# Kernel optimization log

Measured on AMD Instinct MI355X. Metric: run time of the kernel, lower is better.

## Reference

```python
import jax, jax.numpy as jnp
import numpy as np

WS = 512   # window_size
LB = 1     # look_backward
LF = 1     # look_forward
H = 16     # num_attention_heads
NC = LB + LF + 1  # concatenated windows per query window


def _collect(a, pad_value):
    # a: [B, nw, ws, ...]; gather windows [i-LB, i+LF] for each window i,
    # padding the window axis with pad_value (faithful to collect_windows).
    nw = a.shape[1]
    pads = [(0, 0), (LB, LF)] + [(0, 0)] * (a.ndim - 2)
    ap = jnp.pad(a, pads, constant_values=pad_value)
    idx = jnp.arange(nw)[:, None] + jnp.arange(NC)[None, :]  # [nw, NC]
    g = ap[:, idx]  # [B, nw, NC, ws, ...]
    return g.reshape(g.shape[0], nw, NC * a.shape[2], *a.shape[3:])


def setup_inputs() -> dict:
    key = jax.random.key(0)
    ks = jax.random.split(key, 9)
    B, S, E = 1, 4096, 1024
    x = jax.random.normal(ks[0], (B, S, E), dtype=jnp.float32)
    std = 0.02
    wq = std * jax.random.normal(ks[1], (E, E), dtype=jnp.float32)
    wk = std * jax.random.normal(ks[2], (E, E), dtype=jnp.float32)
    wv = std * jax.random.normal(ks[3], (E, E), dtype=jnp.float32)
    wo = std * jax.random.normal(ks[4], (E, E), dtype=jnp.float32)
    bq = std * jax.random.normal(ks[5], (E,), dtype=jnp.float32)
    bk = std * jax.random.normal(ks[6], (E,), dtype=jnp.float32)
    bv = std * jax.random.normal(ks[7], (E,), dtype=jnp.float32)
    bo = std * jax.random.normal(ks[8], (E,), dtype=jnp.float32)
    return {"x": x, "wq": wq, "bq": bq, "wk": wk, "bk": bk,
            "wv": wv, "bv": bv, "wo": wo, "bo": bo}


def reference(x, wq, bq, wk, bk, wv, bv, wo, bo):
    B, S, E = x.shape
    hd = E // H
    nw = S // WS  # seq_len chosen divisible by window_size

    def proj(w, b):
        y = x @ w.T + b
        return y.reshape(B, S, H, hd).transpose(0, 2, 1, 3).reshape(B * H, S, hd)

    q = proj(wq, bq)
    k = proj(wk, bk)
    v = proj(wv, bv)

    qb = q.reshape(B * H, nw, WS, hd)
    # NOTE: original pads K/V window buffers with value -1 (not zero); pad
    # positions are NOT masked (the `!= -1` clause excludes them) -- replicated.
    kb = _collect(k.reshape(B * H, nw, WS, hd), -1.0)  # [BH, nw, NC*WS, hd]
    vb = _collect(v.reshape(B * H, nw, WS, hd), -1.0)

    t = jnp.arange(S, dtype=jnp.int32).reshape(1, nw, WS)
    ct = _collect(t, -1)  # [1, nw, NC*WS] key positions (-1 for pads)

    # Unscaled QK^T (original applies no 1/sqrt(d)).
    scores = jnp.einsum('bwqd,bwkd->bwqk', qb, kb)  # [BH, nw, WS, NC*WS]

    qi = t.reshape(1, nw, WS, 1)          # query absolute positions
    ctb = ct[:, :, None, :]               # key absolute positions
    over = ((ctb > qi + WS * LF) | (ctb < qi - WS * LB)) & (ctb != -1)
    scores = jnp.where(over, -jnp.inf, scores)

    attn = jax.nn.softmax(scores, axis=-1)
    out = jnp.einsum('bwqk,bwkd->bwqd', attn, vb)  # [BH, nw, WS, hd]
    out = out.reshape(B, H, S, hd).transpose(0, 2, 1, 3).reshape(B, S, E)
    return out @ wo.T + bo
```

## Files before the change

### kernel.cpp

```cpp
#include <hip/hip_runtime.h>
#include <stdint.h>

#define S 4096
#define E 1024
#define NH 16
#define HD 64
#define WSZ 512

typedef _Float16 f16x8 __attribute__((ext_vector_type(8)));
typedef _Float16 f16x4 __attribute__((ext_vector_type(4)));
typedef float f32x4 __attribute__((ext_vector_type(4)));
typedef unsigned short u16;
typedef unsigned int u32;

__device__ __forceinline__ u16 f2h_bits(float f) {
    union { _Float16 h; u16 u; } cv; cv.h = (_Float16)f; return cv.u;
}

__device__ __forceinline__ void gld16(const u16* g, u16* l) {
    __builtin_amdgcn_global_load_lds((const __attribute__((address_space(1))) void*)g,
                                     (__attribute__((address_space(3))) void*)l, 16, 0, 0);
}

struct CvtArgs {
    const float* s[5];
    u16* d[5];
    int n[5];
};
__global__ void cvt5(CvtArgs a) {
    int seg = blockIdx.y;
    const float* __restrict__ s = a.s[seg];
    u16* __restrict__ d = a.d[seg];
    int n = a.n[seg];
    for (int i = (blockIdx.x * 256 + threadIdx.x) * 4; i < n; i += gridDim.x * 1024) {
        float4 f = *(const float4*)&s[i];
        uint2 o;
        o.x = (u32)f2h_bits(f.x) | ((u32)f2h_bits(f.y) << 16);
        o.y = (u32)f2h_bits(f.z) | ((u32)f2h_bits(f.w) << 16);
        *(uint2*)&d[i] = o;
    }
}

__global__ __launch_bounds__(256) void gemm_qkv(
    const u16* __restrict__ A, const u16* __restrict__ B,
    u16* __restrict__ OutQK, u16* __restrict__ OutVT,
    const float* __restrict__ b0, const float* __restrict__ b1, const float* __restrict__ b2,
    int K) {
    __shared__ __align__(16) u16 As[128 * 32];
    __shared__ __align__(16) u16 Bs[128 * 32];
    const int tid = threadIdx.x;
    const int wid = tid >> 6, lid = tid & 63, quad = lid >> 4, l16 = lid & 15;
    const int wm = wid >> 1, wn = wid & 1;
    const int bm0 = blockIdx.y * 128, bn0 = blockIdx.x * 128;

    f32x4 acc[4][4] = {};
    const int sr = tid >> 2, sc = (tid & 3) * 8;

    for (int k0 = 0; k0 < K; k0 += 32) {
        __syncthreads();
        gld16(&A[(size_t)(bm0 + sr) * K + k0 + sc],      &As[tid * 8]);
        gld16(&A[(size_t)(bm0 + sr + 64) * K + k0 + sc], &As[2048 + tid * 8]);
        gld16(&B[(size_t)(bn0 + sr) * K + k0 + sc],      &Bs[tid * 8]);
        gld16(&B[(size_t)(bn0 + sr + 64) * K + k0 + sc], &Bs[2048 + tid * 8]);
        __syncthreads();
        f16x8 af[4], bf[4];
#pragma unroll
        for (int i = 0; i < 4; ++i) af[i] = *(const f16x8*)&As[(wm * 64 + i * 16 + l16) * 32 + quad * 8];
#pragma unroll
        for (int j = 0; j < 4; ++j) bf[j] = *(const f16x8*)&Bs[(wn * 64 + j * 16 + l16) * 32 + quad * 8];
#pragma unroll
        for (int i = 0; i < 4; ++i)
#pragma unroll
            for (int j = 0; j < 4; ++j)
                acc[i][j] = __builtin_amdgcn_mfma_f32_16x16x32_f16(af[i], bf[j], acc[i][j], 0, 0, 0);
    }

    const bool isV = (bn0 >= 2048);
#pragma unroll
    for (int j = 0; j < 4; ++j) {
        int n = bn0 + wn * 64 + j * 16 + l16;
        float bias = (n < 1024) ? b0[n] : (n < 2048 ? b1[n - 1024] : b2[n - 2048]);
#pragma unroll
        for (int i = 0; i < 4; ++i) {
            int m0 = bm0 + wm * 64 + i * 16 + quad * 4;
            if (!isV) {
#pragma unroll
                for (int r = 0; r < 4; ++r)
                    OutQK[(size_t)(m0 + r) * 2048 + n] = f2h_bits(acc[i][j][r] + bias);
            } else {
                u16 h0 = f2h_bits(acc[i][j][0] + bias);
                u16 h1 = f2h_bits(acc[i][j][1] + bias);
                u16 h2 = f2h_bits(acc[i][j][2] + bias);
                u16 h3 = f2h_bits(acc[i][j][3] + bias);
                uint2 pk;
                pk.x = (u32)h0 | ((u32)h1 << 16);
                pk.y = (u32)h2 | ((u32)h3 << 16);
                *(uint2*)&OutVT[(size_t)(n - 2048) * 4096 + m0] = pk;
            }
        }
    }
}

__global__ __launch_bounds__(256) void gemm_n64(
    const u16* __restrict__ A, const u16* __restrict__ B, float* __restrict__ OutF,
    const float* __restrict__ bias, int N, int K) {
    __shared__ __align__(16) u16 As[128 * 32];
    __shared__ __align__(16) u16 Bs[64 * 32];
    const int tid = threadIdx.x;
    const int wid = tid >> 6, lid = tid & 63, quad = lid >> 4, l16 = lid & 15;
    const int bm0 = blockIdx.y * 128, bn0 = blockIdx.x * 64;

    f32x4 acc[2][4] = {};
    const int sr = tid >> 2, sc = (tid & 3) * 8;

    for (int k0 = 0; k0 < K; k0 += 32) {
        __syncthreads();
        gld16(&A[(size_t)(bm0 + sr) * K + k0 + sc],      &As[tid * 8]);
        gld16(&A[(size_t)(bm0 + sr + 64) * K + k0 + sc], &As[2048 + tid * 8]);
        gld16(&B[(size_t)(bn0 + sr) * K + k0 + sc],      &Bs[tid * 8]);
        __syncthreads();
        f16x8 af[2], bf[4];
#pragma unroll
        for (int i = 0; i < 2; ++i) af[i] = *(const f16x8*)&As[(wid * 32 + i * 16 + l16) * 32 + quad * 8];
#pragma unroll
        for (int j = 0; j < 4; ++j) bf[j] = *(const f16x8*)&Bs[(j * 16 + l16) * 32 + quad * 8];
#pragma unroll
        for (int i = 0; i < 2; ++i)
#pragma unroll
            for (int j = 0; j < 4; ++j)
                acc[i][j] = __builtin_amdgcn_mfma_f32_16x16x32_f16(af[i], bf[j], acc[i][j], 0, 0, 0);
    }

#pragma unroll
    for (int j = 0; j < 4; ++j) {
        int n = bn0 + j * 16 + l16;
        float bv = bias[n];
#pragma unroll
        for (int i = 0; i < 2; ++i) {
            int m0 = bm0 + wid * 32 + i * 16 + quad * 4;
#pragma unroll
            for (int r = 0; r < 4; ++r)
                OutF[(size_t)(m0 + r) * N + n] = acc[i][j][r] + bv;
        }
    }
}

__global__ __launch_bounds__(512, 4) void attn_win(const u16* __restrict__ QK, const u16* __restrict__ VT,
                                                   u16* __restrict__ AO) {
    const int qt = blockIdx.x, w = blockIdx.y, h = blockIdx.z;
    const int tid = threadIdx.x, wid = tid >> 6, lid = tid & 63, quad = lid >> 4, l16 = lid & 15;

    __shared__ __align__(16) u16 Ks[2][64 * 32];
    __shared__ __align__(16) u16 Vt[2][64 * 36];

    const int qrow = w * WSZ + qt * 128 + wid * 16 + l16;
    f16x8 qf[2];
#pragma unroll
    for (int ks = 0; ks < 2; ++ks)
        qf[ks] = *(const f16x8*)&QK[(size_t)qrow * 2048 + h * 64 + ks * 32 + quad * 8];

    f32x4 oacc[4] = {};
    float mrun = -30000.f;
    float lsum = 0.f;

    const int g0base = (w - 1) * WSZ;
    const int rqloc = qt * 128 + wid * 16 + l16;
    const int rqw0 = qt * 128 + wid * 16;
    const u16 NEG1 = 0xBC00;

    const int kst = tid & 255, kkh = tid >> 8;
    const int vd = tid >> 3, vk0 = (tid & 7) * 8;

    for (int c = 0; c < 24; ++c) {
        const int g0 = g0base + c * 64;
        const bool pad_chunk = (g0 < 0) || (g0 >= S);
        const bool band = (c * 64 + 63 >= qt * 128) && (c * 64 <= qt * 128 + 1151);
        if (!(pad_chunk || band)) continue;

        __syncthreads();
        if (!pad_chunk) {
            gld16(QK + (size_t)(g0 + (kst >> 2)) * 2048 + 1024 + h * 64 + kkh * 32 + (kst & 3) * 8,
                  &Ks[0][0] + kkh * 2048 + kst * 8);
            {
                uint4 va = *(const uint4*)(VT + (size_t)(h * 64 + vd) * 4096 + g0 + vk0);
                u16* vp = &Vt[vk0 >> 5][vd * 36 + (vk0 & 31)];
                *(uint2*)(vp)     = make_uint2(va.x, va.y);
                *(uint2*)(vp + 4) = make_uint2(va.z, va.w);
            }
        } else {
            {
                u32 p = ((u32)NEG1 << 16) | NEG1;
                uint4 val = make_uint4(p, p, p, p);
                *(uint4*)&Ks[kkh][(kst >> 2) * 32 + (kst & 3) * 8] = val;
                u16* vp = &Vt[vk0 >> 5][vd * 36 + (vk0 & 31)];
                *(uint2*)(vp)     = make_uint2(p, p);
                *(uint2*)(vp + 4) = make_uint2(p, p);
            }
        }
        __syncthreads();

        f32x4 sc[4];
#pragma unroll
        for (int nt = 0; nt < 4; ++nt) {
            f16x8 kf0 = *(const f16x8*)&Ks[0][(nt * 16 + l16) * 32 + quad * 8];
            f16x8 kf1 = *(const f16x8*)&Ks[1][(nt * 16 + l16) * 32 + quad * 8];
            f32x4 t = {};
            t = __builtin_amdgcn_mfma_f32_16x16x32_f16(kf0, qf[0], t, 0, 0, 0);
            t = __builtin_amdgcn_mfma_f32_16x16x32_f16(kf1, qf[1], t, 0, 0, 0);
            sc[nt] = t;
        }

        const bool needs_mask = !pad_chunk &&
            ((c * 64 < rqw0 + 16) || (c * 64 + 63 > rqw0 + 1024));
        if (needs_mask) {
#pragma unroll
            for (int nt = 0; nt < 4; ++nt)
#pragma unroll
                for (int r = 0; r < 4; ++r) {
                    int n = c * 64 + nt * 16 + quad * 4 + r;
                    if (n < rqloc || n > rqloc + 1024) sc[nt][r] = -30000.f;
                }
        }

        float mloc = mrun;
#pragma unroll
        for (int nt = 0; nt < 4; ++nt) {
            mloc = fmaxf(mloc, fmaxf(fmaxf(sc[nt][0], sc[nt][1]), fmaxf(sc[nt][2], sc[nt][3])));
        }
        mloc = fmaxf(mloc, __shfl_xor(mloc, 16, 64));
        mloc = fmaxf(mloc, __shfl_xor(mloc, 32, 64));
        float alpha = __expf(mrun - mloc);
        mrun = mloc;
        float ls = 0.f;
        f16x4 pf[4];
#pragma unroll
        for (int nt = 0; nt < 4; ++nt)
#pragma unroll
            for (int r = 0; r < 4; ++r) {
                float p = __expf(sc[nt][r] - mloc);
                ls += p;
                pf[nt][r] = (_Float16)p;
            }
        lsum = lsum * alpha + ls;
        float ao[4];
#pragma unroll
        for (int r = 0; r < 4; ++r) ao[r] = __shfl(alpha, quad * 4 + r, 64);
#pragma unroll
        for (int dt = 0; dt < 4; ++dt)
#pragma unroll
            for (int r = 0; r < 4; ++r) oacc[dt][r] *= ao[r];

#pragma unroll
        for (int nt = 0; nt < 4; ++nt)
#pragma unroll
            for (int dt = 0; dt < 4; ++dt) {
                f16x4 vf = *(const f16x4*)&Vt[nt >> 1][(dt * 16 + l16) * 36 + (nt & 1) * 16 + quad * 4];
                oacc[dt] = __builtin_amdgcn_mfma_f32_16x16x16f16(pf[nt], vf, oacc[dt], 0, 0, 0);
            }
    }

    float lt = lsum;
    lt += __shfl_xor(lt, 16, 64);
    lt += __shfl_xor(lt, 32, 64);
    float linv = 1.f / lt;
    float lrec[4];
#pragma unroll
    for (int r = 0; r < 4; ++r) lrec[r] = __shfl(linv, quad * 4 + r, 64);
#pragma unroll
    for (int dt = 0; dt < 4; ++dt)
#pragma unroll
        for (int r = 0; r < 4; ++r) {
            int srow = w * WSZ + qt * 128 + wid * 16 + quad * 4 + r;
            int col = h * 64 + dt * 16 + l16;
            AO[(size_t)srow * E + col] = f2h_bits(oacc[dt][r] * lrec[r]);
        }
}

extern "C" void kernel_launch(void* const* d_in, const int* in_sizes, int n_in,
                              void* d_out, int out_size, void* d_ws, size_t ws_size,
                              hipStream_t stream) {
    const float* x  = (const float*)d_in[0];
    const float* wq = (const float*)d_in[1];
    const float* bq = (const float*)d_in[2];
    const float* wk = (const float*)d_in[3];
    const float* bk = (const float*)d_in[4];
    const float* wv = (const float*)d_in[5];
    const float* bv = (const float*)d_in[6];
    const float* wo = (const float*)d_in[7];
    const float* bo = (const float*)d_in[8];
    float* out = (float*)d_out;

    char* ws = (char*)d_ws;
    u16* XH  = (u16*)(ws);
    u16* WC  = (u16*)(ws + 8388608);
    u16* WOh = (u16*)(ws + 14680064);
    u16* QK  = (u16*)(ws + 16777216);
    u16* VTg = (u16*)(ws + 33554432);
    u16* AOh = (u16*)(ws + 41943040);

    CvtArgs ca;
    ca.s[0] = x;  ca.d[0] = XH;            ca.n[0] = 4194304;
    ca.s[1] = wq; ca.d[1] = WC;            ca.n[1] = 1048576;
    ca.s[2] = wk; ca.d[2] = WC + 1048576;  ca.n[2] = 1048576;
    ca.s[3] = wv; ca.d[3] = WC + 2097152;  ca.n[3] = 1048576;
    ca.s[4] = wo; ca.d[4] = WOh;           ca.n[4] = 1048576;
    cvt5<<<dim3(1024, 5), 256, 0, stream>>>(ca);

    gemm_qkv<<<dim3(24, 32), 256, 0, stream>>>(XH, WC, QK, VTg, bq, bk, bv, 1024);
    attn_win<<<dim3(4, 8, 16), 512, 0, stream>>>(QK, VTg, AOh);
    gemm_n64<<<dim3(16, 32), 256, 0, stream>>>(AOh, WOh, out, bo, 1024, 1024);
}
```

Before: 202.0 us.

## Handle pad windows analytically, fold log2e into Q, skip rescale, swap GEMM grid order

The attention kernel stops loading and multiplying the constant -1 pad chunks for the edge windows. Their contribution is computed in closed form (score = -sum(q), value = -1, count 512) and merged into the final normalization. Q is pre-scaled by log2(e) so exp2f can replace __expf. The output rescale is skipped when no lane's running max increases. Separately, both GEMM grids are transposed so consecutive blocks walk along M instead of N, which changes L2 reuse. Risks include fp16 rounding from scaling Q in half precision and extra code in the epilogue.

```diff
diff --git a/kernel.cpp b/kernel.cpp
--- a/kernel.cpp
+++ b/kernel.cpp
@@ -51,7 +51,7 @@
     const int tid = threadIdx.x;
     const int wid = tid >> 6, lid = tid & 63, quad = lid >> 4, l16 = lid & 15;
     const int wm = wid >> 1, wn = wid & 1;
-    const int bm0 = blockIdx.y * 128, bn0 = blockIdx.x * 128;
+    const int bm0 = blockIdx.x * 128, bn0 = blockIdx.y * 128;
 
     f32x4 acc[4][4] = {};
     const int sr = tid >> 2, sc = (tid & 3) * 8;
@@ -108,7 +108,7 @@
     __shared__ __align__(16) u16 Bs[64 * 32];
     const int tid = threadIdx.x;
     const int wid = tid >> 6, lid = tid & 63, quad = lid >> 4, l16 = lid & 15;
-    const int bm0 = blockIdx.y * 128, bn0 = blockIdx.x * 64;
+    const int bm0 = blockIdx.x * 128, bn0 = blockIdx.y * 64;
 
     f32x4 acc[2][4] = {};
     const int sr = tid >> 2, sc = (tid & 3) * 8;
@@ -154,10 +154,25 @@
     __shared__ __align__(16) u16 Vt[2][64 * 36];
 
     const int qrow = w * WSZ + qt * 128 + wid * 16 + l16;
+    const _Float16 L2E = (_Float16)1.44269504f;
     f16x8 qf[2];
 #pragma unroll
-    for (int ks = 0; ks < 2; ++ks)
+    for (int ks = 0; ks < 2; ++ks) {
         qf[ks] = *(const f16x8*)&QK[(size_t)qrow * 2048 + h * 64 + ks * 32 + quad * 8];
+#pragma unroll
+        for (int j = 0; j < 8; ++j) qf[ks][j] *= L2E;
+    }
+
+    const int npad = (w == 0 || w == 7) ? 512 : 0;
+    float s_p = 0.f;
+    if (npad) {
+        float sq = 0.f;
+#pragma unroll
+        for (int j = 0; j < 8; ++j) sq += (float)qf[0][j] + (float)qf[1][j];
+        sq += __shfl_xor(sq, 16, 64);
+        sq += __shfl_xor(sq, 32, 64);
+        s_p = -sq;
+    }
 
     f32x4 oacc[4] = {};
     float mrun = -30000.f;
@@ -166,36 +181,23 @@
     const int g0base = (w - 1) * WSZ;
     const int rqloc = qt * 128 + wid * 16 + l16;
     const int rqw0 = qt * 128 + wid * 16;
-    const u16 NEG1 = 0xBC00;
 
     const int kst = tid & 255, kkh = tid >> 8;
     const int vd = tid >> 3, vk0 = (tid & 7) * 8;
 
     for (int c = 0; c < 24; ++c) {
         const int g0 = g0base + c * 64;
-        const bool pad_chunk = (g0 < 0) || (g0 >= S);
-        const bool band = (c * 64 + 63 >= qt * 128) && (c * 64 <= qt * 128 + 1151);
-        if (!(pad_chunk || band)) continue;
-
-        __syncthreads();
-        if (!pad_chunk) {
-            gld16(QK + (size_t)(g0 + (kst >> 2)) * 2048 + 1024 + h * 64 + kkh * 32 + (kst & 3) * 8,
-                  &Ks[0][0] + kkh * 2048 + kst * 8);
-            {
-                uint4 va = *(const uint4*)(VT + (size_t)(h * 64 + vd) * 4096 + g0 + vk0);
-                u16* vp = &Vt[vk0 >> 5][vd * 36 + (vk0 & 31)];
-                *(uint2*)(vp)     = make_uint2(va.x, va.y);
-                *(uint2*)(vp + 4) = make_uint2(va.z, va.w);
-            }
-        } else {
-            {
-                u32 p = ((u32)NEG1 << 16) | NEG1;
-                uint4 val = make_uint4(p, p, p, p);
-                *(uint4*)&Ks[kkh][(kst >> 2) * 32 + (kst & 3) * 8] = val;
-                u16* vp = &Vt[vk0 >> 5][vd * 36 + (vk0 & 31)];
-                *(uint2*)(vp)     = make_uint2(p, p);
-                *(uint2*)(vp + 4) = make_uint2(p, p);
-            }
+        if (g0 < 0 || g0 >= S) continue;
+        if (!((c * 64 + 63 >= qt * 128) && (c * 64 <= qt * 128 + 1151))) continue;
+
+        __syncthreads();
+        gld16(QK + (size_t)(g0 + (kst >> 2)) * 2048 + 1024 + h * 64 + kkh * 32 + (kst & 3) * 8,
+              &Ks[0][0] + kkh * 2048 + kst * 8);
+        {
+            uint4 va = *(const uint4*)(VT + (size_t)(h * 64 + vd) * 4096 + g0 + vk0);
+            u16* vp = &Vt[vk0 >> 5][vd * 36 + (vk0 & 31)];
+            *(uint2*)(vp)     = make_uint2(va.x, va.y);
+            *(uint2*)(vp + 4) = make_uint2(va.z, va.w);
         }
         __syncthreads();
 
@@ -210,8 +212,7 @@
             sc[nt] = t;
         }
 
-        const bool needs_mask = !pad_chunk &&
-            ((c * 64 < rqw0 + 16) || (c * 64 + 63 > rqw0 + 1024));
+        const bool needs_mask = (c * 64 < rqw0 + 16) || (c * 64 + 63 > rqw0 + 1024);
         if (needs_mask) {
 #pragma unroll
             for (int nt = 0; nt < 4; ++nt)
@@ -224,31 +225,36 @@
 
         float mloc = mrun;
 #pragma unroll
-        for (int nt = 0; nt < 4; ++nt) {
+        for (int nt = 0; nt < 4; ++nt)
             mloc = fmaxf(mloc, fmaxf(fmaxf(sc[nt][0], sc[nt][1]), fmaxf(sc[nt][2], sc[nt][3])));
-        }
         mloc = fmaxf(mloc, __shfl_xor(mloc, 16, 64));
         mloc = fmaxf(mloc, __shfl_xor(mloc, 32, 64));
-        float alpha = __expf(mrun - mloc);
-        mrun = mloc;
+
+        const bool up = __any(mloc > mrun);
         float ls = 0.f;
         f16x4 pf[4];
 #pragma unroll
         for (int nt = 0; nt < 4; ++nt)
 #pragma unroll
             for (int r = 0; r < 4; ++r) {
-                float p = __expf(sc[nt][r] - mloc);
+                float p = exp2f(sc[nt][r] - mloc);
                 ls += p;
                 pf[nt][r] = (_Float16)p;
             }
-        lsum = lsum * alpha + ls;
-        float ao[4];
-#pragma unroll
-        for (int r = 0; r < 4; ++r) ao[r] = __shfl(alpha, quad * 4 + r, 64);
-#pragma unroll
-        for (int dt = 0; dt < 4; ++dt)
-#pragma unroll
-            for (int r = 0; r < 4; ++r) oacc[dt][r] *= ao[r];
+        if (up) {
+            float alpha = exp2f(mrun - mloc);
+            mrun = mloc;
+            lsum = lsum * alpha + ls;
+            float ao[4];
+#pragma unroll
+            for (int r = 0; r < 4; ++r) ao[r] = __shfl(alpha, quad * 4 + r, 64);
+#pragma unroll
+            for (int dt = 0; dt < 4; ++dt)
+#pragma unroll
+                for (int r = 0; r < 4; ++r) oacc[dt][r] *= ao[r];
+        } else {
+            lsum += ls;
+        }
 
 #pragma unroll
         for (int nt = 0; nt < 4; ++nt)
@@ -262,17 +268,29 @@
     float lt = lsum;
     lt += __shfl_xor(lt, 16, 64);
     lt += __shfl_xor(lt, 32, 64);
+    float aW = 1.f, pw = 0.f;
+    if (npad) {
+        float mnew = fmaxf(mrun, s_p);
+        aW = exp2f(mrun - mnew);
+        pw = 512.f * exp2f(s_p - mnew);
+        lt = lt * aW + pw;
+    }
     float linv = 1.f / lt;
-    float lrec[4];
-#pragma unroll
-    for (int r = 0; r < 4; ++r) lrec[r] = __shfl(linv, quad * 4 + r, 64);
+    float lrec[4], arow[4], pwrow[4];
+#pragma unroll
+    for (int r = 0; r < 4; ++r) {
+        lrec[r]  = __shfl(linv, quad * 4 + r, 64);
+        arow[r]  = __shfl(aW,   quad * 4 + r, 64);
+        pwrow[r] = __shfl(pw,   quad * 4 + r, 64);
+    }
 #pragma unroll
     for (int dt = 0; dt < 4; ++dt)
 #pragma unroll
         for (int r = 0; r < 4; ++r) {
             int srow = w * WSZ + qt * 128 + wid * 16 + quad * 4 + r;
             int col = h * 64 + dt * 16 + l16;
-            AO[(size_t)srow * E + col] = f2h_bits(oacc[dt][r] * lrec[r]);
+            float o = (oacc[dt][r] * arow[r] - pwrow[r]) * lrec[r];
+            AO[(size_t)srow * E + col] = f2h_bits(o);
         }
 }
 
@@ -306,7 +324,7 @@
     ca.s[4] = wo; ca.d[4] = WOh;           ca.n[4] = 1048576;
     cvt5<<<dim3(1024, 5), 256, 0, stream>>>(ca);
 
-    gemm_qkv<<<dim3(24, 32), 256, 0, stream>>>(XH, WC, QK, VTg, bq, bk, bv, 1024);
+    gemm_qkv<<<dim3(32, 24), 256, 0, stream>>>(XH, WC, QK, VTg, bq, bk, bv, 1024);
     attn_win<<<dim3(4, 8, 16), 512, 0, stream>>>(QK, VTg, AOh);
-    gemm_n64<<<dim3(16, 32), 256, 0, stream>>>(AOh, WOh, out, bo, 1024, 1024);
-}
+    gemm_n64<<<dim3(32, 16), 256, 0, stream>>>(AOh, WOh, out, bo, 1024, 1024);
+}
```

New measurement: 198.1 us. No clear change (-2.0%).
